# Kernel optimization log

Measured on AMD Instinct MI355X. Metric: run time of the kernel, lower is better.

The kernel has to match this reference:

```python
import jax, jax.numpy as jnp
import numpy as np
from jax import lax

H_IMG = 128; W_IMG = 128; C_IN = 200; NCLS = 16
N0 = H_IMG * W_IMG; N1 = 4096; N2 = 1024
K = 16  # neighbors(15) + 1 self loop, as in __init__
EPS = 1e-5
SLOPE = 0.01  # LeakyReLU default


def _leaky(x):
    return jnp.where(x >= 0, x, SLOPE * x)


def _bn1d(H, g, b):
    # BatchNorm1d in training mode: batch stats over node dim
    mu = H.mean(0)
    var = H.var(0)
    return (H - mu) * lax.rsqrt(var + EPS) * g + b


def _bn2d(x, g, b):
    mu = x.mean((0, 2, 3), keepdims=True)
    var = x.var((0, 2, 3), keepdims=True)
    return (x - mu) * lax.rsqrt(var + EPS) * g[None, :, None, None] + b[None, :, None, None]


def _ssconv(x, g, b, pw, pb, dw, db):
    # BN -> 1x1 pointwise conv -> LeakyReLU -> depthwise 5x5 conv -> LeakyReLU
    y = _bn2d(x, g, b)
    y = lax.conv_general_dilated(y, pw, (1, 1), 'SAME', dimension_numbers=('NCHW', 'OIHW', 'NCHW')) + pb[None, :, None, None]
    y = _leaky(y)
    c = dw.shape[0]
    y = lax.conv_general_dilated(y, dw, (1, 1), 'SAME', feature_group_count=c, dimension_numbers=('NCHW', 'OIHW', 'NCHW')) + db[None, :, None, None]
    return _leaky(y)


def _gcn(H, g, b, wt, bt, wo, bo, nbr):
    # GCNLayer_PyG, neighbors>0 branch. nbr: [N, K] neighbor indices (col), center broadcast (row)
    Hn = _bn1d(H, g, b)
    th = Hn @ wt + bt            # [N, 128]
    out = Hn @ wo + bo           # [N, F]
    A = jax.nn.sigmoid(jnp.einsum('nkd,nd->nk', th[nbr], th))  # sigmoid(<theta[col], theta[row]>)
    A = jax.nn.softmax(A, axis=1)                              # softmax over K neighbors
    agg = jnp.einsum('nk,nkf->nf', A, out[nbr])                # weighted neighbor aggregate
    return _leaky(agg), A


def _forward(x, hg, hb, hpw, hpb, hdw, hdb,
             e0_g, e0_b, e0_wt, e0_bt, e0_wo, e0_bo,
             e1_g, e1_b, e1_wt, e1_bt, e1_wo, e1_bo,
             d0_g, d0_b, d0_wt, d0_bt, d0_wo, d0_bo,
             tg, tb, tpw, tpb, tdw, tdb, ws, wb,
             S0, S1, Shat0, Shat1, nbr_a, nbr_b):
    x4 = x.transpose(2, 0, 1)[None]                 # [1, C, H, W]
    h0 = _ssconv(x4, hg, hb, hpw, hpb, hdw, hdb)    # [1, 128, H, W]
    H = h0[0].transpose(1, 2, 0).reshape(N0, -1)    # [N0, 128]
    enc0 = H
    H = Shat0 @ H                                   # pool to [N1, 128]
    H, A0 = _gcn(H, e0_g, e0_b, e0_wt, e0_bt, e0_wo, e0_bo, nbr_a)  # [N1, 64]
    enc1 = H
    H = Shat1 @ H                                   # pool to [N2, 64]
    H, A1 = _gcn(H, e1_g, e1_b, e1_wt, e1_bt, e1_wo, e1_bo, nbr_b)  # [N2, 32]
    # decoder
    H = S1 @ H                                      # unpool [N1, 32]
    H = jnp.concatenate([H, enc1], axis=-1)         # [N1, 96]
    H, Ad = _gcn(H, d0_g, d0_b, d0_wt, d0_bt, d0_wo, d0_bo, nbr_a)  # [N1, 64]
    H = S0 @ H                                      # unpool [N0, 64]
    H = jnp.concatenate([H, enc0], axis=-1)         # [N0, 192]
    t = H.reshape(1, H_IMG, W_IMG, -1).transpose(0, 3, 1, 2)
    f = _ssconv(t, tg, tb, tpw, tpb, tdw, tdb)      # [1, 128, H, W]
    f = f[0].transpose(1, 2, 0).reshape(N0, -1)
    Y = jax.nn.softmax(f @ ws + wb, axis=-1)        # [N0, NCLS]
    return Y


def setup_inputs() -> dict:
    key = jax.random.key(0)
    cnt = [0]
    def rn(shape, s=0.05):
        cnt[0] += 1
        return jax.random.normal(jax.random.fold_in(key, cnt[0]), shape, jnp.float32) * s
    x = rn((H_IMG, W_IMG, C_IN), 1.0)
    # balanced hierarchical assignment matrices (one-hot rows)
    S0 = jnp.zeros((N0, N1), jnp.float32).at[jnp.arange(N0), jnp.arange(N0) // (N0 // N1)].set(1.0)
    S1 = jnp.zeros((N1, N2), jnp.float32).at[jnp.arange(N1), jnp.arange(N1) // (N1 // N2)].set(1.0)
    Shat0 = (S0 / S0.sum(0, keepdims=True)).T
    Shat1 = (S1 / S1.sum(0, keepdims=True)).T
    # positions: pixel grid pooled through Shat (as in HiGCN.__init__)
    gx, gy = jnp.meshgrid(jnp.arange(H_IMG), jnp.arange(W_IMG), indexing='ij')
    pos = jnp.stack([gx, gy], -1).reshape(N0, 2).astype(jnp.float32)
    posA = Shat0 @ pos
    posB = Shat1 @ posA
    def knn(p):
        d = ((p[:, None, :] - p[None, :, :]) ** 2).sum(-1)
        return jnp.argsort(d, axis=1)[:, :K].astype(jnp.int32)  # self included (loop=True)
    nbr_a = knn(posA)  # [N1, K], used by enc0 and dec0
    nbr_b = knn(posB)  # [N2, K], used by enc1
    inp = dict(x=x, S0=S0, S1=S1, Shat0=Shat0, Shat1=Shat1, nbr_a=nbr_a, nbr_b=nbr_b)
    inp.update(hg=jnp.ones(C_IN), hb=jnp.zeros(C_IN), hpw=rn((128, C_IN, 1, 1)),
               hpb=jnp.zeros(128), hdw=rn((128, 1, 5, 5)), hdb=jnp.zeros(128))
    for tag, ci, co in (('e0', 128, 64), ('e1', 64, 32), ('d0', 96, 64)):
        inp[tag + '_g'] = jnp.ones(ci); inp[tag + '_b'] = jnp.zeros(ci)
        inp[tag + '_wt'] = rn((ci, 128)); inp[tag + '_bt'] = jnp.zeros(128)
        inp[tag + '_wo'] = rn((ci, co)); inp[tag + '_bo'] = jnp.zeros(co)
    inp.update(tg=jnp.ones(192), tb=jnp.zeros(192), tpw=rn((128, 192, 1, 1)),
               tpb=jnp.zeros(128), tdw=rn((128, 1, 5, 5)), tdb=jnp.zeros(128))
    inp.update(ws=rn((128, NCLS)), wb=jnp.zeros(NCLS))
    return inp


def reference(x, hg, hb, hpw, hpb, hdw, hdb,
              e0_g, e0_b, e0_wt, e0_bt, e0_wo, e0_bo,
              e1_g, e1_b, e1_wt, e1_bt, e1_wo, e1_bo,
              d0_g, d0_b, d0_wt, d0_bt, d0_wo, d0_bo,
              tg, tb, tpw, tpb, tdw, tdb, ws, wb,
              S0, S1, Shat0, Shat1, nbr_a, nbr_b):
    return _forward(x, hg, hb, hpw, hpb, hdw, hdb,
                    e0_g, e0_b, e0_wt, e0_bt, e0_wo, e0_bo,
                    e1_g, e1_b, e1_wt, e1_bt, e1_wo, e1_bo,
                    d0_g, d0_b, d0_wt, d0_bt, d0_wo, d0_bo,
                    tg, tb, tpw, tpb, tdw, tdb, ws, wb,
                    S0, S1, Shat0, Shat1, nbr_a, nbr_b)
```

## Files before the change

kernel.cpp:

```cpp
#include <hip/hip_runtime.h>
#include <hip/hip_bf16.h>
#include <math.h>

using bf16 = __hip_bfloat16;

#define H_IMG 128
#define W_IMG 128
#define C_IN  200
#define NCLS  16
#define N0    16384
#define N1    4096
#define N2    1024
#define KNB   16
#define EPS   1e-5f
#define SLOPE 0.01f

__device__ __forceinline__ float ldf(const float* p, long i) { return p[i]; }
__device__ __forceinline__ float ldf(const bf16* p, long i) { return __bfloat162float(p[i]); }
__device__ __forceinline__ float leaky(float v) { return v >= 0.f ? v : SLOPE * v; }

__global__ void detect_kernel(const unsigned short* __restrict__ x, int* __restrict__ flag) {
    if (threadIdx.x != 0 || blockIdx.x != 0) return;
    int cnt = 0;
    for (int i = 0; i < 4096; i++) {
        unsigned short e = (unsigned short)((x[i] >> 7) & 0xFF);
        if (e >= 0xC0) cnt++;
    }
    *flag = (cnt > 32) ? 1 : 0;
}

template <typename TX, typename TW>
__device__ __forceinline__ void bn_stats_body(const TX* __restrict__ X, int P, int C,
                                              const TW* __restrict__ g, const TW* __restrict__ b,
                                              float* __restrict__ alpha, float* __restrict__ beta) {
    int c = blockIdx.x;
    int t = threadIdx.x;
    float s = 0.f, s2 = 0.f;
    for (int p = t; p < P; p += 256) {
        float v = ldf(X, (long)p * C + c);
        s += v; s2 += v * v;
    }
    __shared__ float rs[256], rq[256];
    rs[t] = s; rq[t] = s2; __syncthreads();
    for (int k = 128; k > 0; k >>= 1) {
        if (t < k) { rs[t] += rs[t + k]; rq[t] += rq[t + k]; }
        __syncthreads();
    }
    if (t == 0) {
        float mu = rs[0] / (float)P;
        float var = rq[0] / (float)P - mu * mu;
        float a = rsqrtf(var + EPS) * ldf(g, c);
        alpha[c] = a;
        beta[c] = ldf(b, c) - mu * a;
    }
}

__global__ __launch_bounds__(256) void bn_stats_kernel(const void* X, int P, int C,
                                                       const void* g, const void* b,
                                                       float* alpha, float* beta,
                                                       const int* flag, int xraw) {
    if (*flag) bn_stats_body<float, float>((const float*)X, P, C, (const float*)g, (const float*)b, alpha, beta);
    else if (xraw) bn_stats_body<bf16, bf16>((const bf16*)X, P, C, (const bf16*)g, (const bf16*)b, alpha, beta);
    else bn_stats_body<float, bf16>((const float*)X, P, C, (const bf16*)g, (const bf16*)b, alpha, beta);
}

template <typename TW>
__device__ __forceinline__ void fold_body(const TW* __restrict__ W, const TW* __restrict__ bias,
                                          const float* __restrict__ alpha, const float* __restrict__ beta,
                                          float* __restrict__ Wf, float* __restrict__ Bf,
                                          int Ci, int Co, int omajor) {
    int j = blockIdx.x;
    int t = threadIdx.x;
    float acc = 0.f;
    for (int c = t; c < Ci; c += 256) {
        float w = omajor ? ldf(W, (long)j * Ci + c) : ldf(W, (long)c * Co + j);
        Wf[(long)c * Co + j] = w * alpha[c];
        acc += w * beta[c];
    }
    __shared__ float red[256];
    red[t] = acc; __syncthreads();
    for (int k = 128; k > 0; k >>= 1) { if (t < k) red[t] += red[t + k]; __syncthreads(); }
    if (t == 0) Bf[j] = ldf(bias, (long)j) + red[0];
}

__global__ __launch_bounds__(256) void fold_kernel(const void* W, const void* bias,
                                                   const float* alpha, const float* beta,
                                                   float* Wf, float* Bf, int Ci, int Co, int omajor,
                                                   const int* flag) {
    if (*flag) fold_body<float>((const float*)W, (const float*)bias, alpha, beta, Wf, Bf, Ci, Co, omajor);
    else fold_body<bf16>((const bf16*)W, (const bf16*)bias, alpha, beta, Wf, Bf, Ci, Co, omajor);
}

template <typename T, int ACT>
__device__ __forceinline__ void gemm_body(const T* __restrict__ In, const float* __restrict__ Wf,
                                          const float* __restrict__ Bf, float* __restrict__ Out,
                                          int Ci, int Co) {
    int tid = blockIdx.x * 256 + threadIdx.x;
    int n = tid / Co;
    int j = tid - n * Co;
    const T* in = In + (long)n * Ci;
    float acc = Bf[j];
#pragma unroll 4
    for (int c = 0; c < Ci; c++) acc += ldf(in, (long)c) * Wf[(long)c * Co + j];
    if (ACT) acc = leaky(acc);
    Out[(long)n * Co + j] = acc;
}

__global__ __launch_bounds__(256) void gemm_dyn_kernel(const void* In, const float* Wf, const float* Bf,
                                                       float* Out, int Ci, int Co, const int* flag) {
    if (*flag) gemm_body<float, 1>((const float*)In, Wf, Bf, Out, Ci, Co);
    else gemm_body<bf16, 1>((const bf16*)In, Wf, Bf, Out, Ci, Co);
}

template <int ACT>
__global__ __launch_bounds__(256) void gemm_f32_kernel(const float* In, const float* Wf, const float* Bf,
                                                       float* Out, int Ci, int Co) {
    gemm_body<float, ACT>(In, Wf, Bf, Out, Ci, Co);
}

template <typename TW>
__device__ __forceinline__ void dw_body(const float* __restrict__ In, const TW* __restrict__ dwp,
                                        const TW* __restrict__ dbp, float* __restrict__ Out) {
    int tid = blockIdx.x * 256 + threadIdx.x;
    int o = tid & 127;
    int p = tid >> 7;
    int h = p >> 7, w = p & 127;
    float wr[25];
#pragma unroll
    for (int i = 0; i < 25; i++) wr[i] = ldf(dwp, (long)o * 25 + i);
    float acc = ldf(dbp, (long)o);
#pragma unroll
    for (int dh = -2; dh <= 2; dh++) {
        int hh = h + dh;
        if ((unsigned)hh >= (unsigned)H_IMG) continue;
#pragma unroll
        for (int dv = -2; dv <= 2; dv++) {
            int ww = w + dv;
            if ((unsigned)ww >= (unsigned)W_IMG) continue;
            acc += In[(long)(((hh << 7) + ww) << 7) + o] * wr[(dh + 2) * 5 + (dv + 2)];
        }
    }
    Out[tid] = leaky(acc);
}

__global__ __launch_bounds__(256) void dw_kernel(const float* In, const void* dwp, const void* dbp,
                                                 float* Out, const int* flag) {
    if (*flag) dw_body<float>(In, (const float*)dwp, (const float*)dbp, Out);
    else dw_body<bf16>(In, (const bf16*)dwp, (const bf16*)dbp, Out);
}

__global__ __launch_bounds__(256) void pool4_kernel(const float* __restrict__ In, float* __restrict__ Out, int F) {
    int tid = blockIdx.x * 256 + threadIdx.x;
    int j = tid / F;
    int f = tid - j * F;
    const float* base = In + (long)(4 * j) * F + f;
    Out[tid] = 0.25f * (base[0] + base[F] + base[2 * F] + base[3 * F]);
}

__global__ __launch_bounds__(64) void attn_kernel(const float* __restrict__ th, const float* __restrict__ outm,
                                                  const int* __restrict__ nbr, float* __restrict__ dst, int co) {
    int n = blockIdx.x;
    int l = threadIdx.x;
    float r0 = th[(long)n * 128 + l];
    float r1 = th[(long)n * 128 + 64 + l];
    int mk[KNB];
    float av[KNB];
#pragma unroll
    for (int k = 0; k < KNB; k++) {
        int m = nbr[n * KNB + k];
        mk[k] = m;
        float v = r0 * th[(long)m * 128 + l] + r1 * th[(long)m * 128 + 64 + l];
#pragma unroll
        for (int off = 32; off > 0; off >>= 1) v += __shfl_xor(v, off, 64);
        av[k] = 1.f / (1.f + expf(-v));
    }
    float amax = av[0];
#pragma unroll
    for (int k = 1; k < KNB; k++) amax = fmaxf(amax, av[k]);
    float den = 0.f;
#pragma unroll
    for (int k = 0; k < KNB; k++) { av[k] = expf(av[k] - amax); den += av[k]; }
    float rden = 1.f / den;
    if (l < co) {
        float acc = 0.f;
#pragma unroll
        for (int k = 0; k < KNB; k++) acc += av[k] * outm[(long)mk[k] * co + l];
        dst[(long)n * co + l] = leaky(acc * rden);
    }
}

__global__ __launch_bounds__(256) void concat_hcat_kernel(const float* __restrict__ Hd, const float* __restrict__ enc1,
                                                          float* __restrict__ Hcat) {
    int tid = blockIdx.x * 256 + threadIdx.x;
    int n = tid / 96;
    int f = tid - n * 96;
    Hcat[tid] = (f < 32) ? Hd[(long)(n >> 2) * 32 + f] : enc1[(long)n * 64 + (f - 32)];
}

__global__ __launch_bounds__(256) void concat_g_kernel(const float* __restrict__ Hdec, const float* __restrict__ H0,
                                                       float* __restrict__ G) {
    int tid = blockIdx.x * 256 + threadIdx.x;
    int p = tid / 192;
    int f = tid - p * 192;
    G[tid] = (f < 64) ? Hdec[(long)(p >> 2) * 64 + f] : H0[(long)p * 128 + (f - 64)];
}

template <typename TW>
__device__ __forceinline__ void cls_body(const float* __restrict__ F, const TW* __restrict__ wsw,
                                         const TW* __restrict__ wb, TW* __restrict__ out) {
    int tid = blockIdx.x * 256 + threadIdx.x;
    int p = tid >> 4;
    int j = tid & 15;
    float acc = ldf(wb, (long)j);
#pragma unroll 4
    for (int c = 0; c < 128; c++) acc += F[(long)p * 128 + c] * ldf(wsw, (long)c * 16 + j);
    float m = acc;
#pragma unroll
    for (int s = 8; s > 0; s >>= 1) m = fmaxf(m, __shfl_xor(m, s, 16));
    float e = expf(acc - m);
    float d = e;
#pragma unroll
    for (int s = 8; s > 0; s >>= 1) d += __shfl_xor(d, s, 16);
    float r = e / d;
    if constexpr (sizeof(TW) == 2) out[tid] = __float2bfloat16(r);
    else out[tid] = r;
}

__global__ __launch_bounds__(256) void cls_kernel(const float* F, const void* wsw, const void* wb,
                                                  void* out, const int* flag) {
    if (*flag) cls_body<float>(F, (const float*)wsw, (const float*)wb, (float*)out);
    else cls_body<bf16>(F, (const bf16*)wsw, (const bf16*)wb, (bf16*)out);
}

extern "C" void kernel_launch(void* const* d_in, const int* in_sizes, int n_in,
                              void* d_out, int out_size, void* d_ws, size_t ws_size,
                              hipStream_t stream) {
    bool dict = (in_sizes[1] > 1000000);
    int I_x, I_nbr_a, I_nbr_b, I_hg, I_ws, I_e0, I_e1, I_d0, I_tg;
    if (dict) {
        I_x = 0; I_nbr_a = 5; I_nbr_b = 6; I_hg = 7; I_e0 = 13; I_e1 = 19; I_d0 = 25; I_tg = 31; I_ws = 37;
    } else {
        I_x = 0; I_hg = 1; I_e0 = 7; I_e1 = 13; I_d0 = 19; I_tg = 25; I_ws = 31; I_nbr_a = 37; I_nbr_b = 38;
    }
    const void* x    = d_in[I_x];
    const int* nbr_a = (const int*)d_in[I_nbr_a];
    const int* nbr_b = (const int*)d_in[I_nbr_b];
    const void* hg   = d_in[I_hg + 0];
    const void* hb   = d_in[I_hg + 1];
    const void* hpw  = d_in[I_hg + 2];
    const void* hpb  = d_in[I_hg + 3];
    const void* hdw  = d_in[I_hg + 4];
    const void* hdb  = d_in[I_hg + 5];
    const void* e0_g = d_in[I_e0 + 0];
    const void* e0_b = d_in[I_e0 + 1];
    const void* e0_wt= d_in[I_e0 + 2];
    const void* e0_bt= d_in[I_e0 + 3];
    const void* e0_wo= d_in[I_e0 + 4];
    const void* e0_bo= d_in[I_e0 + 5];
    const void* e1_g = d_in[I_e1 + 0];
    const void* e1_b = d_in[I_e1 + 1];
    const void* e1_wt= d_in[I_e1 + 2];
    const void* e1_bt= d_in[I_e1 + 3];
    const void* e1_wo= d_in[I_e1 + 4];
    const void* e1_bo= d_in[I_e1 + 5];
    const void* d0_g = d_in[I_d0 + 0];
    const void* d0_b = d_in[I_d0 + 1];
    const void* d0_wt= d_in[I_d0 + 2];
    const void* d0_bt= d_in[I_d0 + 3];
    const void* d0_wo= d_in[I_d0 + 4];
    const void* d0_bo= d_in[I_d0 + 5];
    const void* tg   = d_in[I_tg + 0];
    const void* tb   = d_in[I_tg + 1];
    const void* tpw  = d_in[I_tg + 2];
    const void* tpb  = d_in[I_tg + 3];
    const void* tdw  = d_in[I_tg + 4];
    const void* tdb  = d_in[I_tg + 5];
    const void* wsw  = d_in[I_ws + 0];
    const void* wb   = d_in[I_ws + 1];

    float* W = (float*)d_ws;
    float* AB_a  = W + 0;
    float* AB_b  = W + 256;
    float* WF1   = W + 512;
    float* BF1   = W + 33280;
    float* WF2   = W + 33536;
    float* BF2   = W + 41728;
    int*   dflag = (int*)(W + 49152);
    float* R0    = W + 65536;
    float* R1    = R0 + (long)N0*192;
    float* H1b   = R1 + (long)N0*128;
    float* THb   = H1b + (long)N1*128;
    float* OUTb  = THb + (long)N1*128;
    float* ENC1  = OUTb + (long)N1*64;
    float* H2b   = ENC1 + (long)N1*64;
    float* HDb   = H2b + (long)N2*64;
    float* HCAT  = HDb + (long)N2*32;
    float* HDEC  = HCAT + (long)N1*96;

    detect_kernel<<<1, 64, 0, stream>>>((const unsigned short*)x, dflag);

    bn_stats_kernel<<<C_IN, 256, 0, stream>>>(x, N0, C_IN, hg, hb, AB_a, AB_b, dflag, 1);
    fold_kernel<<<128, 256, 0, stream>>>(hpw, hpb, AB_a, AB_b, WF1, BF1, C_IN, 128, 1, dflag);
    gemm_dyn_kernel<<<(N0 * 128) / 256, 256, 0, stream>>>(x, WF1, BF1, R0, C_IN, 128, dflag);
    dw_kernel<<<(N0 * 128) / 256, 256, 0, stream>>>(R0, hdw, hdb, R1, dflag);
    pool4_kernel<<<(N1 * 128) / 256, 256, 0, stream>>>(R1, H1b, 128);

    bn_stats_kernel<<<128, 256, 0, stream>>>(H1b, N1, 128, e0_g, e0_b, AB_a, AB_b, dflag, 0);
    fold_kernel<<<128, 256, 0, stream>>>(e0_wt, e0_bt, AB_a, AB_b, WF1, BF1, 128, 128, 0, dflag);
    fold_kernel<<<64, 256, 0, stream>>>(e0_wo, e0_bo, AB_a, AB_b, WF2, BF2, 128, 64, 0, dflag);
    gemm_f32_kernel<0><<<(N1 * 128) / 256, 256, 0, stream>>>(H1b, WF1, BF1, THb, 128, 128);
    gemm_f32_kernel<0><<<(N1 * 64) / 256, 256, 0, stream>>>(H1b, WF2, BF2, OUTb, 128, 64);
    attn_kernel<<<N1, 64, 0, stream>>>(THb, OUTb, nbr_a, ENC1, 64);
    pool4_kernel<<<(N2 * 64) / 256, 256, 0, stream>>>(ENC1, H2b, 64);

    bn_stats_kernel<<<64, 256, 0, stream>>>(H2b, N2, 64, e1_g, e1_b, AB_a, AB_b, dflag, 0);
    fold_kernel<<<128, 256, 0, stream>>>(e1_wt, e1_bt, AB_a, AB_b, WF1, BF1, 64, 128, 0, dflag);
    fold_kernel<<<32, 256, 0, stream>>>(e1_wo, e1_bo, AB_a, AB_b, WF2, BF2, 64, 32, 0, dflag);
    gemm_f32_kernel<0><<<(N2 * 128) / 256, 256, 0, stream>>>(H2b, WF1, BF1, THb, 64, 128);
    gemm_f32_kernel<0><<<(N2 * 32) / 256, 256, 0, stream>>>(H2b, WF2, BF2, OUTb, 64, 32);
    attn_kernel<<<N2, 64, 0, stream>>>(THb, OUTb, nbr_b, HDb, 32);

    concat_hcat_kernel<<<(N1 * 96) / 256, 256, 0, stream>>>(HDb, ENC1, HCAT);
    bn_stats_kernel<<<96, 256, 0, stream>>>(HCAT, N1, 96, d0_g, d0_b, AB_a, AB_b, dflag, 0);
    fold_kernel<<<128, 256, 0, stream>>>(d0_wt, d0_bt, AB_a, AB_b, WF1, BF1, 96, 128, 0, dflag);
    fold_kernel<<<64, 256, 0, stream>>>(d0_wo, d0_bo, AB_a, AB_b, WF2, BF2, 96, 64, 0, dflag);
    gemm_f32_kernel<0><<<(N1 * 128) / 256, 256, 0, stream>>>(HCAT, WF1, BF1, THb, 96, 128);
    gemm_f32_kernel<0><<<(N1 * 64) / 256, 256, 0, stream>>>(HCAT, WF2, BF2, OUTb, 96, 64);
    attn_kernel<<<N1, 64, 0, stream>>>(THb, OUTb, nbr_a, HDEC, 64);

    concat_g_kernel<<<(N0 * 192) / 256, 256, 0, stream>>>(HDEC, R1, R0);
    bn_stats_kernel<<<192, 256, 0, stream>>>(R0, N0, 192, tg, tb, AB_a, AB_b, dflag, 0);
    fold_kernel<<<128, 256, 0, stream>>>(tpw, tpb, AB_a, AB_b, WF1, BF1, 192, 128, 1, dflag);
    gemm_f32_kernel<1><<<(N0 * 128) / 256, 256, 0, stream>>>(R0, WF1, BF1, R1, 192, 128);
    dw_kernel<<<(N0 * 128) / 256, 256, 0, stream>>>(R1, tdw, tdb, R0, dflag);
    cls_kernel<<<(N0 * NCLS) / 256, 256, 0, stream>>>(R0, wsw, wb, d_out, dflag);
}
```

Measured before the change: 1.042 ms.

## Fuse whole HiGCN pipeline into one cooperative persistent kernel with grid syncs

```diff
diff --git a/kernel.cpp b/kernel.cpp
--- a/kernel.cpp
+++ b/kernel.cpp
@@ -1,7 +1,9 @@
 #include <hip/hip_runtime.h>
 #include <hip/hip_bf16.h>
+#include <hip/hip_cooperative_groups.h>
 #include <math.h>
 
+namespace cg = cooperative_groups;
 using bf16 = __hip_bfloat16;
 
 #define H_IMG 128
@@ -15,221 +17,355 @@
 #define EPS   1e-5f
 #define SLOPE 0.01f
 
-__device__ __forceinline__ float ldf(const float* p, long i) { return p[i]; }
-__device__ __forceinline__ float ldf(const bf16* p, long i) { return __bfloat162float(p[i]); }
+#define NBLK  512
+#define NTHR  256
+#define GSZ   (NBLK * NTHR)
+
 __device__ __forceinline__ float leaky(float v) { return v >= 0.f ? v : SLOPE * v; }
-
-__global__ void detect_kernel(const unsigned short* __restrict__ x, int* __restrict__ flag) {
-    if (threadIdx.x != 0 || blockIdx.x != 0) return;
-    int cnt = 0;
-    for (int i = 0; i < 4096; i++) {
-        unsigned short e = (unsigned short)((x[i] >> 7) & 0xFF);
-        if (e >= 0xC0) cnt++;
-    }
-    *flag = (cnt > 32) ? 1 : 0;
-}
-
-template <typename TX, typename TW>
-__device__ __forceinline__ void bn_stats_body(const TX* __restrict__ X, int P, int C,
-                                              const TW* __restrict__ g, const TW* __restrict__ b,
-                                              float* __restrict__ alpha, float* __restrict__ beta) {
-    int c = blockIdx.x;
-    int t = threadIdx.x;
+__device__ __forceinline__ float lda(const void* p, long i, bool F32) {
+    return F32 ? ((const float*)p)[i] : __bfloat162float(((const bf16*)p)[i]);
+}
+
+struct Params {
+    const void *x; const int *nbr_a, *nbr_b;
+    const void *hg,*hb,*hpw,*hpb,*hdw,*hdb;
+    const void *e0_g,*e0_b,*e0_wt,*e0_bt,*e0_wo,*e0_bo;
+    const void *e1_g,*e1_b,*e1_wt,*e1_bt,*e1_wo,*e1_bo;
+    const void *d0_g,*d0_b,*d0_wt,*d0_bt,*d0_wo,*d0_bo;
+    const void *tg,*tb,*tpw,*tpb,*tdw,*tdb,*wsw,*wb;
+    void* out; float* W;
+};
+
+__device__ __forceinline__ void stats_dev(const float* X, long ld, long col, int P, int rep, int Pv,
+                                          const void* g, const void* bb, float* alpha, float* beta,
+                                          int c, int t, float* smA, float* smB, bool F32) {
     float s = 0.f, s2 = 0.f;
-    for (int p = t; p < P; p += 256) {
-        float v = ldf(X, (long)p * C + c);
-        s += v; s2 += v * v;
-    }
-    __shared__ float rs[256], rq[256];
-    rs[t] = s; rq[t] = s2; __syncthreads();
-    for (int k = 128; k > 0; k >>= 1) {
-        if (t < k) { rs[t] += rs[t + k]; rq[t] += rq[t + k]; }
-        __syncthreads();
-    }
+    for (int r = t; r < P; r += NTHR) { float v = X[(long)r * ld + col]; s += v; s2 += v * v; }
+    smA[t] = s; smB[t] = s2; __syncthreads();
+    for (int k = 128; k > 0; k >>= 1) { if (t < k) { smA[t] += smA[t + k]; smB[t] += smB[t + k]; } __syncthreads(); }
     if (t == 0) {
-        float mu = rs[0] / (float)P;
-        float var = rq[0] / (float)P - mu * mu;
-        float a = rsqrtf(var + EPS) * ldf(g, c);
-        alpha[c] = a;
-        beta[c] = ldf(b, c) - mu * a;
-    }
-}
-
-__global__ __launch_bounds__(256) void bn_stats_kernel(const void* X, int P, int C,
-                                                       const void* g, const void* b,
-                                                       float* alpha, float* beta,
-                                                       const int* flag, int xraw) {
-    if (*flag) bn_stats_body<float, float>((const float*)X, P, C, (const float*)g, (const float*)b, alpha, beta);
-    else if (xraw) bn_stats_body<bf16, bf16>((const bf16*)X, P, C, (const bf16*)g, (const bf16*)b, alpha, beta);
-    else bn_stats_body<float, bf16>((const float*)X, P, C, (const bf16*)g, (const bf16*)b, alpha, beta);
-}
-
-template <typename TW>
-__device__ __forceinline__ void fold_body(const TW* __restrict__ W, const TW* __restrict__ bias,
-                                          const float* __restrict__ alpha, const float* __restrict__ beta,
-                                          float* __restrict__ Wf, float* __restrict__ Bf,
-                                          int Ci, int Co, int omajor) {
-    int j = blockIdx.x;
-    int t = threadIdx.x;
+        float fr = (float)rep / (float)Pv;
+        float mu = smA[0] * fr;
+        float var = smB[0] * fr - mu * mu;
+        float a = rsqrtf(var + EPS) * lda(g, c, F32);
+        alpha[c] = a; beta[c] = lda(bb, c, F32) - mu * a;
+    }
+    __syncthreads();
+}
+
+__device__ __forceinline__ void fold_dev(const void* Wsrc, const void* bias,
+                                         const float* alpha, const float* beta,
+                                         float* Wf, float* Bf, int Ci, int Co, int omajor,
+                                         int j, int t, float* sm, bool F32) {
     float acc = 0.f;
-    for (int c = t; c < Ci; c += 256) {
-        float w = omajor ? ldf(W, (long)j * Ci + c) : ldf(W, (long)c * Co + j);
+    for (int c = t; c < Ci; c += NTHR) {
+        float w = lda(Wsrc, omajor ? (long)j * Ci + c : (long)c * Co + j, F32);
         Wf[(long)c * Co + j] = w * alpha[c];
         acc += w * beta[c];
     }
-    __shared__ float red[256];
-    red[t] = acc; __syncthreads();
-    for (int k = 128; k > 0; k >>= 1) { if (t < k) red[t] += red[t + k]; __syncthreads(); }
-    if (t == 0) Bf[j] = ldf(bias, (long)j) + red[0];
-}
-
-__global__ __launch_bounds__(256) void fold_kernel(const void* W, const void* bias,
-                                                   const float* alpha, const float* beta,
-                                                   float* Wf, float* Bf, int Ci, int Co, int omajor,
-                                                   const int* flag) {
-    if (*flag) fold_body<float>((const float*)W, (const float*)bias, alpha, beta, Wf, Bf, Ci, Co, omajor);
-    else fold_body<bf16>((const bf16*)W, (const bf16*)bias, alpha, beta, Wf, Bf, Ci, Co, omajor);
-}
-
-template <typename T, int ACT>
-__device__ __forceinline__ void gemm_body(const T* __restrict__ In, const float* __restrict__ Wf,
-                                          const float* __restrict__ Bf, float* __restrict__ Out,
-                                          int Ci, int Co) {
-    int tid = blockIdx.x * 256 + threadIdx.x;
-    int n = tid / Co;
-    int j = tid - n * Co;
-    const T* in = In + (long)n * Ci;
-    float acc = Bf[j];
-#pragma unroll 4
-    for (int c = 0; c < Ci; c++) acc += ldf(in, (long)c) * Wf[(long)c * Co + j];
-    if (ACT) acc = leaky(acc);
-    Out[(long)n * Co + j] = acc;
-}
-
-__global__ __launch_bounds__(256) void gemm_dyn_kernel(const void* In, const float* Wf, const float* Bf,
-                                                       float* Out, int Ci, int Co, const int* flag) {
-    if (*flag) gemm_body<float, 1>((const float*)In, Wf, Bf, Out, Ci, Co);
-    else gemm_body<bf16, 1>((const bf16*)In, Wf, Bf, Out, Ci, Co);
-}
-
-template <int ACT>
-__global__ __launch_bounds__(256) void gemm_f32_kernel(const float* In, const float* Wf, const float* Bf,
-                                                       float* Out, int Ci, int Co) {
-    gemm_body<float, ACT>(In, Wf, Bf, Out, Ci, Co);
-}
-
-template <typename TW>
-__device__ __forceinline__ void dw_body(const float* __restrict__ In, const TW* __restrict__ dwp,
-                                        const TW* __restrict__ dbp, float* __restrict__ Out) {
-    int tid = blockIdx.x * 256 + threadIdx.x;
-    int o = tid & 127;
-    int p = tid >> 7;
-    int h = p >> 7, w = p & 127;
+    sm[t] = acc; __syncthreads();
+    for (int k = 128; k > 0; k >>= 1) { if (t < k) sm[t] += sm[t + k]; __syncthreads(); }
+    if (t == 0) Bf[j] = lda(bias, j, F32) + sm[0];
+    __syncthreads();
+}
+
+__device__ __forceinline__ void attn_dev(const float* th, const float* outm, const int* nbr,
+                                         float* dst, int co, int Nn, int gtid) {
+    int lane = gtid & 63;
+    int wv = gtid >> 6;
+    const int nw = GSZ >> 6;
+    for (int n = wv; n < Nn; n += nw) {
+        float r0 = th[(long)n * 128 + lane];
+        float r1 = th[(long)n * 128 + 64 + lane];
+        int mk[KNB]; float av[KNB];
+#pragma unroll
+        for (int k = 0; k < KNB; k++) {
+            int m = nbr[n * KNB + k]; mk[k] = m;
+            float v = r0 * th[(long)m * 128 + lane] + r1 * th[(long)m * 128 + 64 + lane];
+#pragma unroll
+            for (int off = 32; off > 0; off >>= 1) v += __shfl_xor(v, off, 64);
+            av[k] = 1.f / (1.f + expf(-v));
+        }
+        float amax = av[0];
+#pragma unroll
+        for (int k = 1; k < KNB; k++) amax = fmaxf(amax, av[k]);
+        float den = 0.f;
+#pragma unroll
+        for (int k = 0; k < KNB; k++) { av[k] = expf(av[k] - amax); den += av[k]; }
+        float rden = 1.f / den;
+        if (lane < co) {
+            float acc = 0.f;
+#pragma unroll
+            for (int k = 0; k < KNB; k++) acc += av[k] * outm[(long)mk[k] * co + lane];
+            dst[(long)n * co + lane] = leaky(acc * rden);
+        }
+    }
+}
+
+__device__ __forceinline__ void dw_dev(const float* In, const void* wsrc, const void* bsrc,
+                                       float* Out, int gtid, bool F32) {
+    int o = gtid & 127;
     float wr[25];
 #pragma unroll
-    for (int i = 0; i < 25; i++) wr[i] = ldf(dwp, (long)o * 25 + i);
-    float acc = ldf(dbp, (long)o);
-#pragma unroll
-    for (int dh = -2; dh <= 2; dh++) {
-        int hh = h + dh;
-        if ((unsigned)hh >= (unsigned)H_IMG) continue;
-#pragma unroll
-        for (int dv = -2; dv <= 2; dv++) {
-            int ww = w + dv;
-            if ((unsigned)ww >= (unsigned)W_IMG) continue;
-            acc += In[(long)(((hh << 7) + ww) << 7) + o] * wr[(dh + 2) * 5 + (dv + 2)];
-        }
-    }
-    Out[tid] = leaky(acc);
-}
-
-__global__ __launch_bounds__(256) void dw_kernel(const float* In, const void* dwp, const void* dbp,
-                                                 float* Out, const int* flag) {
-    if (*flag) dw_body<float>(In, (const float*)dwp, (const float*)dbp, Out);
-    else dw_body<bf16>(In, (const bf16*)dwp, (const bf16*)dbp, Out);
-}
-
-__global__ __launch_bounds__(256) void pool4_kernel(const float* __restrict__ In, float* __restrict__ Out, int F) {
-    int tid = blockIdx.x * 256 + threadIdx.x;
-    int j = tid / F;
-    int f = tid - j * F;
-    const float* base = In + (long)(4 * j) * F + f;
-    Out[tid] = 0.25f * (base[0] + base[F] + base[2 * F] + base[3 * F]);
-}
-
-__global__ __launch_bounds__(64) void attn_kernel(const float* __restrict__ th, const float* __restrict__ outm,
-                                                  const int* __restrict__ nbr, float* __restrict__ dst, int co) {
-    int n = blockIdx.x;
-    int l = threadIdx.x;
-    float r0 = th[(long)n * 128 + l];
-    float r1 = th[(long)n * 128 + 64 + l];
-    int mk[KNB];
-    float av[KNB];
-#pragma unroll
-    for (int k = 0; k < KNB; k++) {
-        int m = nbr[n * KNB + k];
-        mk[k] = m;
-        float v = r0 * th[(long)m * 128 + l] + r1 * th[(long)m * 128 + 64 + l];
-#pragma unroll
-        for (int off = 32; off > 0; off >>= 1) v += __shfl_xor(v, off, 64);
-        av[k] = 1.f / (1.f + expf(-v));
-    }
-    float amax = av[0];
-#pragma unroll
-    for (int k = 1; k < KNB; k++) amax = fmaxf(amax, av[k]);
-    float den = 0.f;
-#pragma unroll
-    for (int k = 0; k < KNB; k++) { av[k] = expf(av[k] - amax); den += av[k]; }
-    float rden = 1.f / den;
-    if (l < co) {
-        float acc = 0.f;
-#pragma unroll
-        for (int k = 0; k < KNB; k++) acc += av[k] * outm[(long)mk[k] * co + l];
-        dst[(long)n * co + l] = leaky(acc * rden);
-    }
-}
-
-__global__ __launch_bounds__(256) void concat_hcat_kernel(const float* __restrict__ Hd, const float* __restrict__ enc1,
-                                                          float* __restrict__ Hcat) {
-    int tid = blockIdx.x * 256 + threadIdx.x;
-    int n = tid / 96;
-    int f = tid - n * 96;
-    Hcat[tid] = (f < 32) ? Hd[(long)(n >> 2) * 32 + f] : enc1[(long)n * 64 + (f - 32)];
-}
-
-__global__ __launch_bounds__(256) void concat_g_kernel(const float* __restrict__ Hdec, const float* __restrict__ H0,
-                                                       float* __restrict__ G) {
-    int tid = blockIdx.x * 256 + threadIdx.x;
-    int p = tid / 192;
-    int f = tid - p * 192;
-    G[tid] = (f < 64) ? Hdec[(long)(p >> 2) * 64 + f] : H0[(long)p * 128 + (f - 64)];
-}
-
-template <typename TW>
-__device__ __forceinline__ void cls_body(const float* __restrict__ F, const TW* __restrict__ wsw,
-                                         const TW* __restrict__ wb, TW* __restrict__ out) {
-    int tid = blockIdx.x * 256 + threadIdx.x;
-    int p = tid >> 4;
-    int j = tid & 15;
-    float acc = ldf(wb, (long)j);
-#pragma unroll 4
-    for (int c = 0; c < 128; c++) acc += F[(long)p * 128 + c] * ldf(wsw, (long)c * 16 + j);
-    float m = acc;
-#pragma unroll
-    for (int s = 8; s > 0; s >>= 1) m = fmaxf(m, __shfl_xor(m, s, 16));
-    float e = expf(acc - m);
-    float d = e;
-#pragma unroll
-    for (int s = 8; s > 0; s >>= 1) d += __shfl_xor(d, s, 16);
-    float r = e / d;
-    if constexpr (sizeof(TW) == 2) out[tid] = __float2bfloat16(r);
-    else out[tid] = r;
-}
-
-__global__ __launch_bounds__(256) void cls_kernel(const float* F, const void* wsw, const void* wb,
-                                                  void* out, const int* flag) {
-    if (*flag) cls_body<float>(F, (const float*)wsw, (const float*)wb, (float*)out);
-    else cls_body<bf16>(F, (const bf16*)wsw, (const bf16*)wb, (bf16*)out);
+    for (int i = 0; i < 25; i++) wr[i] = lda(wsrc, (long)o * 25 + i, F32);
+    float bias = lda(bsrc, (long)o, F32);
+    for (long e = gtid; e < (long)N0 * 128; e += GSZ) {
+        int pp = (int)(e >> 7);
+        int h = pp >> 7, w = pp & 127;
+        float acc = bias;
+#pragma unroll
+        for (int dh = -2; dh <= 2; dh++) {
+            int hh = h + dh;
+            if ((unsigned)hh >= (unsigned)H_IMG) continue;
+#pragma unroll
+            for (int dv = -2; dv <= 2; dv++) {
+                int ww = w + dv;
+                if ((unsigned)ww >= (unsigned)W_IMG) continue;
+                acc += In[(long)(((hh << 7) + ww) << 7) + o] * wr[(dh + 2) * 5 + (dv + 2)];
+            }
+        }
+        Out[e] = leaky(acc);
+    }
+}
+
+__global__ __launch_bounds__(NTHR) void higcn_fused(Params p) {
+    cg::grid_group grid = cg::this_grid();
+    const int t = threadIdx.x, b = blockIdx.x;
+    const int gtid = b * NTHR + t;
+    __shared__ float sA[NTHR], sB[NTHR];
+
+    float* W = p.W;
+    int*   dflag = (int*)W;
+    float* AB_a = W + 256;
+    float* AB_b = W + 512;
+    float* WF1  = W + 1024;
+    float* BF1  = W + 33792;
+    float* WF2  = W + 34048;
+    float* BF2  = W + 42240;
+    float* R0   = W + 65536;
+    float* R1   = R0 + (long)N0*128;
+    float* H1   = R1 + (long)N0*128;
+    float* TH   = H1 + (long)N1*128;
+    float* OU   = TH + (long)N1*128;
+    float* E1   = OU + (long)N1*64;
+    float* H2   = E1 + (long)N1*64;
+    float* HD   = H2 + (long)N2*64;
+    float* HDE  = HD + (long)N2*32;
+
+    if (b == 0) {
+        const unsigned short* u = (const unsigned short*)p.x;
+        int cnt = 0;
+        for (int i = t; i < 4096; i += NTHR) { unsigned e = (u[i] >> 7) & 0xFF; cnt += (e >= 0xC0); }
+        sA[t] = (float)cnt; __syncthreads();
+        for (int k = 128; k > 0; k >>= 1) { if (t < k) sA[t] += sA[t + k]; __syncthreads(); }
+        if (t == 0) { dflag[0] = (sA[0] > 32.f) ? 1 : 0; __threadfence(); }
+    }
+    grid.sync();
+    const bool F32 = (dflag[0] != 0);
+
+    if (b < C_IN) {
+        float s = 0.f, s2 = 0.f;
+        if (F32) {
+            const float* X = (const float*)p.x;
+            for (int r = t; r < N0; r += NTHR) { float v = X[(long)r * C_IN + b]; s += v; s2 += v * v; }
+        } else {
+            const bf16* X = (const bf16*)p.x;
+            for (int r = t; r < N0; r += NTHR) { float v = __bfloat162float(X[(long)r * C_IN + b]); s += v; s2 += v * v; }
+        }
+        sA[t] = s; sB[t] = s2; __syncthreads();
+        for (int k = 128; k > 0; k >>= 1) { if (t < k) { sA[t] += sA[t + k]; sB[t] += sB[t + k]; } __syncthreads(); }
+        if (t == 0) {
+            float mu = sA[0] / (float)N0;
+            float var = sB[0] / (float)N0 - mu * mu;
+            float a = rsqrtf(var + EPS) * lda(p.hg, b, F32);
+            AB_a[b] = a; AB_b[b] = lda(p.hb, b, F32) - mu * a;
+        }
+    }
+    grid.sync();
+
+    if (b < 128) fold_dev(p.hpw, p.hpb, AB_a, AB_b, WF1, BF1, C_IN, 128, 1, b, t, sA, F32);
+    grid.sync();
+
+    if (F32) {
+        const float* X = (const float*)p.x;
+        for (long i = gtid; i < (long)N0 * 128; i += GSZ) {
+            int n = (int)(i >> 7), j = (int)(i & 127);
+            const float* in = X + (long)n * C_IN;
+            float acc = BF1[j];
+#pragma unroll 4
+            for (int c = 0; c < C_IN; c++) acc += in[c] * WF1[(long)c * 128 + j];
+            R0[i] = leaky(acc);
+        }
+    } else {
+        const bf16* X = (const bf16*)p.x;
+        for (long i = gtid; i < (long)N0 * 128; i += GSZ) {
+            int n = (int)(i >> 7), j = (int)(i & 127);
+            const bf16* in = X + (long)n * C_IN;
+            float acc = BF1[j];
+#pragma unroll 4
+            for (int c = 0; c < C_IN; c++) acc += __bfloat162float(in[c]) * WF1[(long)c * 128 + j];
+            R0[i] = leaky(acc);
+        }
+    }
+    grid.sync();
+
+    dw_dev(R0, p.hdw, p.hdb, R1, gtid, F32);
+    grid.sync();
+
+    for (long i = gtid; i < (long)N1 * 128; i += GSZ) {
+        int n = (int)(i >> 7), f = (int)(i & 127);
+        const float* base = R1 + (long)(4 * n) * 128 + f;
+        H1[i] = 0.25f * (base[0] + base[128] + base[256] + base[384]);
+    }
+    grid.sync();
+
+    if (b < 128) stats_dev(H1, 128, b, N1, 1, N1, p.e0_g, p.e0_b, AB_a, AB_b, b, t, sA, sB, F32);
+    grid.sync();
+
+    if (b < 128) fold_dev(p.e0_wt, p.e0_bt, AB_a, AB_b, WF1, BF1, 128, 128, 0, b, t, sA, F32);
+    else if (b < 192) fold_dev(p.e0_wo, p.e0_bo, AB_a, AB_b, WF2, BF2, 128, 64, 0, b - 128, t, sA, F32);
+    grid.sync();
+
+    for (long i = gtid; i < (long)N1 * 128; i += GSZ) {
+        int n = (int)(i >> 7), j = (int)(i & 127);
+        const float* in = H1 + (long)n * 128;
+        float acc = BF1[j];
+#pragma unroll 4
+        for (int c = 0; c < 128; c++) acc += in[c] * WF1[(long)c * 128 + j];
+        TH[i] = acc;
+    }
+    for (long i = gtid; i < (long)N1 * 64; i += GSZ) {
+        int n = (int)(i >> 6), j = (int)(i & 63);
+        const float* in = H1 + (long)n * 128;
+        float acc = BF2[j];
+#pragma unroll 4
+        for (int c = 0; c < 128; c++) acc += in[c] * WF2[(long)c * 64 + j];
+        OU[i] = acc;
+    }
+    grid.sync();
+
+    attn_dev(TH, OU, p.nbr_a, E1, 64, N1, gtid);
+    grid.sync();
+
+    for (long i = gtid; i < (long)N2 * 64; i += GSZ) {
+        int n = (int)(i >> 6), f = (int)(i & 63);
+        const float* base = E1 + (long)(4 * n) * 64 + f;
+        H2[i] = 0.25f * (base[0] + base[64] + base[128] + base[192]);
+    }
+    grid.sync();
+
+    if (b < 64) stats_dev(H2, 64, b, N2, 1, N2, p.e1_g, p.e1_b, AB_a, AB_b, b, t, sA, sB, F32);
+    grid.sync();
+
+    if (b < 128) fold_dev(p.e1_wt, p.e1_bt, AB_a, AB_b, WF1, BF1, 64, 128, 0, b, t, sA, F32);
+    else if (b < 160) fold_dev(p.e1_wo, p.e1_bo, AB_a, AB_b, WF2, BF2, 64, 32, 0, b - 128, t, sA, F32);
+    grid.sync();
+
+    for (long i = gtid; i < (long)N2 * 128; i += GSZ) {
+        int n = (int)(i >> 7), j = (int)(i & 127);
+        const float* in = H2 + (long)n * 64;
+        float acc = BF1[j];
+#pragma unroll 4
+        for (int c = 0; c < 64; c++) acc += in[c] * WF1[(long)c * 128 + j];
+        TH[i] = acc;
+    }
+    for (long i = gtid; i < (long)N2 * 32; i += GSZ) {
+        int n = (int)(i >> 5), j = (int)(i & 31);
+        const float* in = H2 + (long)n * 64;
+        float acc = BF2[j];
+#pragma unroll 4
+        for (int c = 0; c < 64; c++) acc += in[c] * WF2[(long)c * 32 + j];
+        OU[i] = acc;
+    }
+    grid.sync();
+
+    attn_dev(TH, OU, p.nbr_b, HD, 32, N2, gtid);
+    grid.sync();
+
+    if (b < 32) stats_dev(HD, 32, b, N2, 4, N1, p.d0_g, p.d0_b, AB_a, AB_b, b, t, sA, sB, F32);
+    else if (b < 96) stats_dev(E1, 64, b - 32, N1, 1, N1, p.d0_g, p.d0_b, AB_a, AB_b, b, t, sA, sB, F32);
+    grid.sync();
+
+    if (b < 128) fold_dev(p.d0_wt, p.d0_bt, AB_a, AB_b, WF1, BF1, 96, 128, 0, b, t, sA, F32);
+    else if (b < 192) fold_dev(p.d0_wo, p.d0_bo, AB_a, AB_b, WF2, BF2, 96, 64, 0, b - 128, t, sA, F32);
+    grid.sync();
+
+    for (long i = gtid; i < (long)N1 * 128; i += GSZ) {
+        int n = (int)(i >> 7), j = (int)(i & 127);
+        const float* hd = HD + (long)(n >> 2) * 32;
+        const float* e1 = E1 + (long)n * 64;
+        float acc = BF1[j];
+#pragma unroll
+        for (int c = 0; c < 32; c++) acc += hd[c] * WF1[(long)c * 128 + j];
+#pragma unroll 4
+        for (int c = 0; c < 64; c++) acc += e1[c] * WF1[(long)(c + 32) * 128 + j];
+        TH[i] = acc;
+    }
+    for (long i = gtid; i < (long)N1 * 64; i += GSZ) {
+        int n = (int)(i >> 6), j = (int)(i & 63);
+        const float* hd = HD + (long)(n >> 2) * 32;
+        const float* e1 = E1 + (long)n * 64;
+        float acc = BF2[j];
+#pragma unroll
+        for (int c = 0; c < 32; c++) acc += hd[c] * WF2[(long)c * 64 + j];
+#pragma unroll 4
+        for (int c = 0; c < 64; c++) acc += e1[c] * WF2[(long)(c + 32) * 64 + j];
+        OU[i] = acc;
+    }
+    grid.sync();
+
+    attn_dev(TH, OU, p.nbr_a, HDE, 64, N1, gtid);
+    grid.sync();
+
+    if (b < 64) stats_dev(HDE, 64, b, N1, 4, N0, p.tg, p.tb, AB_a, AB_b, b, t, sA, sB, F32);
+    else if (b < 192) stats_dev(R1, 128, b - 64, N0, 1, N0, p.tg, p.tb, AB_a, AB_b, b, t, sA, sB, F32);
+    grid.sync();
+
+    if (b < 128) fold_dev(p.tpw, p.tpb, AB_a, AB_b, WF1, BF1, 192, 128, 1, b, t, sA, F32);
+    grid.sync();
+
+    for (long i = gtid; i < (long)N0 * 128; i += GSZ) {
+        int n = (int)(i >> 7), j = (int)(i & 127);
+        const float* hd = HDE + (long)(n >> 2) * 64;
+        const float* h0 = R1 + (long)n * 128;
+        float acc = BF1[j];
+#pragma unroll 4
+        for (int c = 0; c < 64; c++) acc += hd[c] * WF1[(long)c * 128 + j];
+#pragma unroll 4
+        for (int c = 0; c < 128; c++) acc += h0[c] * WF1[(long)(c + 64) * 128 + j];
+        R0[i] = leaky(acc);
+    }
+    grid.sync();
+
+    dw_dev(R0, p.tdw, p.tdb, R1, gtid, F32);
+    grid.sync();
+
+    for (long i = gtid; i < (long)N0 * NCLS; i += GSZ) {
+        int pp = (int)(i >> 4), j = (int)(i & 15);
+        const float* Fv = R1 + (long)pp * 128;
+        float acc;
+        if (F32) {
+            const float* wsw = (const float*)p.wsw;
+            acc = ((const float*)p.wb)[j];
+#pragma unroll 4
+            for (int c = 0; c < 128; c++) acc += Fv[c] * wsw[c * 16 + j];
+        } else {
+            const bf16* wsw = (const bf16*)p.wsw;
+            acc = __bfloat162float(((const bf16*)p.wb)[j]);
+#pragma unroll 4
+            for (int c = 0; c < 128; c++) acc += Fv[c] * __bfloat162float(wsw[c * 16 + j]);
+        }
+        float m = acc;
+#pragma unroll
+        for (int s = 8; s > 0; s >>= 1) m = fmaxf(m, __shfl_xor(m, s, 16));
+        float e = expf(acc - m);
+        float d = e;
+#pragma unroll
+        for (int s = 8; s > 0; s >>= 1) d += __shfl_xor(d, s, 16);
+        float r = e / d;
+        if (F32) ((float*)p.out)[i] = r;
+        else ((bf16*)p.out)[i] = __float2bfloat16(r);
+    }
 }
 
 extern "C" void kernel_launch(void* const* d_in, const int* in_sizes, int n_in,
@@ -242,96 +378,24 @@
     } else {
         I_x = 0; I_hg = 1; I_e0 = 7; I_e1 = 13; I_d0 = 19; I_tg = 25; I_ws = 31; I_nbr_a = 37; I_nbr_b = 38;
     }
-    const void* x    = d_in[I_x];
-    const int* nbr_a = (const int*)d_in[I_nbr_a];
-    const int* nbr_b = (const int*)d_in[I_nbr_b];
-    const void* hg   = d_in[I_hg + 0];
-    const void* hb   = d_in[I_hg + 1];
-    const void* hpw  = d_in[I_hg + 2];
-    const void* hpb  = d_in[I_hg + 3];
-    const void* hdw  = d_in[I_hg + 4];
-    const void* hdb  = d_in[I_hg + 5];
-    const void* e0_g = d_in[I_e0 + 0];
-    const void* e0_b = d_in[I_e0 + 1];
-    const void* e0_wt= d_in[I_e0 + 2];
-    const void* e0_bt= d_in[I_e0 + 3];
-    const void* e0_wo= d_in[I_e0 + 4];
-    const void* e0_bo= d_in[I_e0 + 5];
-    const void* e1_g = d_in[I_e1 + 0];
-    const void* e1_b = d_in[I_e1 + 1];
-    const void* e1_wt= d_in[I_e1 + 2];
-    const void* e1_bt= d_in[I_e1 + 3];
-    const void* e1_wo= d_in[I_e1 + 4];
-    const void* e1_bo= d_in[I_e1 + 5];
-    const void* d0_g = d_in[I_d0 + 0];
-    const void* d0_b = d_in[I_d0 + 1];
-    const void* d0_wt= d_in[I_d0 + 2];
-    const void* d0_bt= d_in[I_d0 + 3];
-    const void* d0_wo= d_in[I_d0 + 4];
-    const void* d0_bo= d_in[I_d0 + 5];
-    const void* tg   = d_in[I_tg + 0];
-    const void* tb   = d_in[I_tg + 1];
-    const void* tpw  = d_in[I_tg + 2];
-    const void* tpb  = d_in[I_tg + 3];
-    const void* tdw  = d_in[I_tg + 4];
-    const void* tdb  = d_in[I_tg + 5];
-    const void* wsw  = d_in[I_ws + 0];
-    const void* wb   = d_in[I_ws + 1];
-
-    float* W = (float*)d_ws;
-    float* AB_a  = W + 0;
-    float* AB_b  = W + 256;
-    float* WF1   = W + 512;
-    float* BF1   = W + 33280;
-    float* WF2   = W + 33536;
-    float* BF2   = W + 41728;
-    int*   dflag = (int*)(W + 49152);
-    float* R0    = W + 65536;
-    float* R1    = R0 + (long)N0*192;
-    float* H1b   = R1 + (long)N0*128;
-    float* THb   = H1b + (long)N1*128;
-    float* OUTb  = THb + (long)N1*128;
-    float* ENC1  = OUTb + (long)N1*64;
-    float* H2b   = ENC1 + (long)N1*64;
-    float* HDb   = H2b + (long)N2*64;
-    float* HCAT  = HDb + (long)N2*32;
-    float* HDEC  = HCAT + (long)N1*96;
-
-    detect_kernel<<<1, 64, 0, stream>>>((const unsigned short*)x, dflag);
-
-    bn_stats_kernel<<<C_IN, 256, 0, stream>>>(x, N0, C_IN, hg, hb, AB_a, AB_b, dflag, 1);
-    fold_kernel<<<128, 256, 0, stream>>>(hpw, hpb, AB_a, AB_b, WF1, BF1, C_IN, 128, 1, dflag);
-    gemm_dyn_kernel<<<(N0 * 128) / 256, 256, 0, stream>>>(x, WF1, BF1, R0, C_IN, 128, dflag);
-    dw_kernel<<<(N0 * 128) / 256, 256, 0, stream>>>(R0, hdw, hdb, R1, dflag);
-    pool4_kernel<<<(N1 * 128) / 256, 256, 0, stream>>>(R1, H1b, 128);
-
-    bn_stats_kernel<<<128, 256, 0, stream>>>(H1b, N1, 128, e0_g, e0_b, AB_a, AB_b, dflag, 0);
-    fold_kernel<<<128, 256, 0, stream>>>(e0_wt, e0_bt, AB_a, AB_b, WF1, BF1, 128, 128, 0, dflag);
-    fold_kernel<<<64, 256, 0, stream>>>(e0_wo, e0_bo, AB_a, AB_b, WF2, BF2, 128, 64, 0, dflag);
-    gemm_f32_kernel<0><<<(N1 * 128) / 256, 256, 0, stream>>>(H1b, WF1, BF1, THb, 128, 128);
-    gemm_f32_kernel<0><<<(N1 * 64) / 256, 256, 0, stream>>>(H1b, WF2, BF2, OUTb, 128, 64);
-    attn_kernel<<<N1, 64, 0, stream>>>(THb, OUTb, nbr_a, ENC1, 64);
-    pool4_kernel<<<(N2 * 64) / 256, 256, 0, stream>>>(ENC1, H2b, 64);
-
-    bn_stats_kernel<<<64, 256, 0, stream>>>(H2b, N2, 64, e1_g, e1_b, AB_a, AB_b, dflag, 0);
-    fold_kernel<<<128, 256, 0, stream>>>(e1_wt, e1_bt, AB_a, AB_b, WF1, BF1, 64, 128, 0, dflag);
-    fold_kernel<<<32, 256, 0, stream>>>(e1_wo, e1_bo, AB_a, AB_b, WF2, BF2, 64, 32, 0, dflag);
-    gemm_f32_kernel<0><<<(N2 * 128) / 256, 256, 0, stream>>>(H2b, WF1, BF1, THb, 64, 128);
-    gemm_f32_kernel<0><<<(N2 * 32) / 256, 256, 0, stream>>>(H2b, WF2, BF2, OUTb, 64, 32);
-    attn_kernel<<<N2, 64, 0, stream>>>(THb, OUTb, nbr_b, HDb, 32);
-
-    concat_hcat_kernel<<<(N1 * 96) / 256, 256, 0, stream>>>(HDb, ENC1, HCAT);
-    bn_stats_kernel<<<96, 256, 0, stream>>>(HCAT, N1, 96, d0_g, d0_b, AB_a, AB_b, dflag, 0);
-    fold_kernel<<<128, 256, 0, stream>>>(d0_wt, d0_bt, AB_a, AB_b, WF1, BF1, 96, 128, 0, dflag);
-    fold_kernel<<<64, 256, 0, stream>>>(d0_wo, d0_bo, AB_a, AB_b, WF2, BF2, 96, 64, 0, dflag);
-    gemm_f32_kernel<0><<<(N1 * 128) / 256, 256, 0, stream>>>(HCAT, WF1, BF1, THb, 96, 128);
-    gemm_f32_kernel<0><<<(N1 * 64) / 256, 256, 0, stream>>>(HCAT, WF2, BF2, OUTb, 96, 64);
-    attn_kernel<<<N1, 64, 0, stream>>>(THb, OUTb, nbr_a, HDEC, 64);
-
-    concat_g_kernel<<<(N0 * 192) / 256, 256, 0, stream>>>(HDEC, R1, R0);
-    bn_stats_kernel<<<192, 256, 0, stream>>>(R0, N0, 192, tg, tb, AB_a, AB_b, dflag, 0);
-    fold_kernel<<<128, 256, 0, stream>>>(tpw, tpb, AB_a, AB_b, WF1, BF1, 192, 128, 1, dflag);
-    gemm_f32_kernel<1><<<(N0 * 128) / 256, 256, 0, stream>>>(R0, WF1, BF1, R1, 192, 128);
-    dw_kernel<<<(N0 * 128) / 256, 256, 0, stream>>>(R1, tdw, tdb, R0, dflag);
-    cls_kernel<<<(N0 * NCLS) / 256, 256, 0, stream>>>(R0, wsw, wb, d_out, dflag);
-}
+    Params prm;
+    prm.x = d_in[I_x];
+    prm.nbr_a = (const int*)d_in[I_nbr_a];
+    prm.nbr_b = (const int*)d_in[I_nbr_b];
+    prm.hg = d_in[I_hg + 0]; prm.hb = d_in[I_hg + 1]; prm.hpw = d_in[I_hg + 2];
+    prm.hpb = d_in[I_hg + 3]; prm.hdw = d_in[I_hg + 4]; prm.hdb = d_in[I_hg + 5];
+    prm.e0_g = d_in[I_e0 + 0]; prm.e0_b = d_in[I_e0 + 1]; prm.e0_wt = d_in[I_e0 + 2];
+    prm.e0_bt = d_in[I_e0 + 3]; prm.e0_wo = d_in[I_e0 + 4]; prm.e0_bo = d_in[I_e0 + 5];
+    prm.e1_g = d_in[I_e1 + 0]; prm.e1_b = d_in[I_e1 + 1]; prm.e1_wt = d_in[I_e1 + 2];
+    prm.e1_bt = d_in[I_e1 + 3]; prm.e1_wo = d_in[I_e1 + 4]; prm.e1_bo = d_in[I_e1 + 5];
+    prm.d0_g = d_in[I_d0 + 0]; prm.d0_b = d_in[I_d0 + 1]; prm.d0_wt = d_in[I_d0 + 2];
+    prm.d0_bt = d_in[I_d0 + 3]; prm.d0_wo = d_in[I_d0 + 4]; prm.d0_bo = d_in[I_d0 + 5];
+    prm.tg = d_in[I_tg + 0]; prm.tb = d_in[I_tg + 1]; prm.tpw = d_in[I_tg + 2];
+    prm.tpb = d_in[I_tg + 3]; prm.tdw = d_in[I_tg + 4]; prm.tdb = d_in[I_tg + 5];
+    prm.wsw = d_in[I_ws + 0]; prm.wb = d_in[I_ws + 1];
+    prm.out = d_out;
+    prm.W = (float*)d_ws;
+
+    void* args[] = { (void*)&prm };
+    hipLaunchCooperativeKernel((const void*)higcn_fused, dim3(NBLK), dim3(NTHR), args, 0, stream);
+}
```

Measured after the change: 2.409 ms. 131% more time.
